# Performance work log

Measured on AMD Instinct MI355X. Metric: run time of the kernel, lower is better.

## Reference

```python
import jax, jax.numpy as jnp
import numpy as np

EMBED_DIM = 1024
NUM_HEADS = 16
D_K = EMBED_DIM // NUM_HEADS


def setup_inputs() -> dict:
    key = jax.random.key(0)
    ks = jax.random.split(key, 5)
    x = jax.random.normal(ks[0], (2, 2048, EMBED_DIM), dtype=jnp.float32)
    # kaiming_normal on 2D params: std = sqrt(2/fan_in) with fan_in = in_features
    w_qkv = jax.random.normal(ks[1], (3 * EMBED_DIM, EMBED_DIM), dtype=jnp.float32) * np.sqrt(2.0 / EMBED_DIM)
    b_qkv = jnp.zeros((3 * EMBED_DIM,), dtype=jnp.float32)
    w_o = jax.random.normal(ks[2], (EMBED_DIM, EMBED_DIM), dtype=jnp.float32) * np.sqrt(2.0 / EMBED_DIM)
    b_o = jnp.zeros((EMBED_DIM,), dtype=jnp.float32)
    return {"x": x, "w_qkv": w_qkv, "b_qkv": b_qkv, "w_o": w_o, "b_o": b_o}


def reference(x, w_qkv, b_qkv, w_o, b_o):
    B, N, C = x.shape
    qkv = x @ w_qkv.T + b_qkv  # [B,N,3C]
    q, k, v = jnp.split(qkv, 3, axis=-1)
    # [B,H,N,d_k]
    q = q.reshape(B, N, NUM_HEADS, D_K).transpose(0, 2, 1, 3)
    k = k.reshape(B, N, NUM_HEADS, D_K).transpose(0, 2, 1, 3)
    v = v.reshape(B, N, NUM_HEADS, D_K).transpose(0, 2, 1, 3)
    # NOTE: original forward scales by 1/sqrt(embed_dim), not 1/sqrt(d_k)
    scores = jnp.einsum('bhqd,bhkd->bhqk', q, k) / np.sqrt(C).astype(np.float32)
    causal = jnp.tril(jnp.ones((N, N), dtype=bool))
    scores = jnp.where(causal, scores, -jnp.inf)
    attn = jax.nn.softmax(scores, axis=-1)
    out = jnp.einsum('bhqk,bhkd->bhqd', attn, v)  # [B,H,N,d_k]
    out = out.transpose(0, 2, 1, 3).reshape(B, N, C)
    return out @ w_o.T + b_o
```

## Files before the change

kernel.cpp:

```cpp
#include <hip/hip_runtime.h>
#include <hip/hip_bf16.h>
#include <math.h>

typedef __bf16 bf16_t;
typedef __bf16 bf16x8 __attribute__((ext_vector_type(8)));
typedef __bf16 bf16x4 __attribute__((ext_vector_type(4)));
typedef __bf16 bf16x2 __attribute__((ext_vector_type(2)));
typedef float f32x4 __attribute__((ext_vector_type(4)));
typedef unsigned u32x4 __attribute__((ext_vector_type(4)));

#define SCALE_L2E 0.045084234f
#define ROUND_B 0.0028169f

#define MFMA16(a, b, c) __builtin_amdgcn_mfma_f32_16x16x32_bf16(a, b, c, 0, 0, 0)

__device__ __forceinline__ unsigned pack2(float a, float b) {
  return __builtin_amdgcn_perm(__builtin_bit_cast(unsigned, b),
                               __builtin_bit_cast(unsigned, a), 0x07060302u);
}

__global__ void convert3_f32_bf16(const float* __restrict__ a, int na,
                                  const float* __restrict__ b, int nb,
                                  const float* __restrict__ c, int nc,
                                  bf16_t* __restrict__ oa, bf16_t* __restrict__ ob,
                                  bf16_t* __restrict__ oc) {
  int i = (blockIdx.x * blockDim.x + threadIdx.x) * 8;
  const float* src;
  bf16_t* dst;
  int off;
  if (i < na) { src = a; dst = oa; off = i; }
  else if (i < na + nb) { src = b; dst = ob; off = i - na; }
  else if (i < na + nb + nc) { src = c; dst = oc; off = i - na - nb; }
  else return;
  float4 u = *(const float4*)&src[off];
  float4 v = *(const float4*)&src[off + 4];
  bf16x8 w = {(bf16_t)u.x, (bf16_t)u.y, (bf16_t)u.z, (bf16_t)u.w,
              (bf16_t)v.x, (bf16_t)v.y, (bf16_t)v.z, (bf16_t)v.w};
  *(bf16x8*)&dst[off] = w;
}

#define GLOBAL_AS __attribute__((address_space(1)))
#define LDS_AS __attribute__((address_space(3)))
__device__ __forceinline__ void g2l16(const void* g, void* l) {
  __builtin_amdgcn_global_load_lds((const GLOBAL_AS void*)g, (LDS_AS void*)l,
                                   16, 0, 0);
}

template <typename TC, int BN>
__launch_bounds__(256)
__global__ void gemm_bt_bias(const bf16_t* __restrict__ A,
                             const bf16_t* __restrict__ B,
                             const float* __restrict__ bias,
                             TC* __restrict__ C,
                             int M, int N, int K) {
  constexpr int NT = BN / 32;
  __shared__ bf16_t As[128 * 32];
  __shared__ bf16_t Bs[BN * 32];

  const int t = threadIdx.x;
  const int wave = t >> 6, lane = t & 63, quad = lane >> 4, ln = lane & 15;
  const int wm = (wave >> 1) * 64, wn = (wave & 1) * (BN / 2);
  const int m0 = blockIdx.y * 128, n0 = blockIdx.x * BN;

  const int srow = lane >> 2;
  const int schunk = ((lane & 3) ^ ((lane >> 3) & 3)) * 8;
  const bf16_t* gA0 = &A[(size_t)(m0 + wave * 32 + srow) * K + schunk];
  const bf16_t* gA1 = gA0 + (size_t)16 * K;
  bf16_t* lA0 = &As[(wave * 32) * 32];
  bf16_t* lA1 = &As[(wave * 32 + 16) * 32];
  const bf16_t* gB0 = &B[(size_t)(n0 + (BN == 128 ? wave * 32 : wave * 16) + srow) * K + schunk];
  const bf16_t* gB1 = gB0 + (size_t)16 * K;
  bf16_t* lB0 = &Bs[((BN == 128 ? wave * 32 : wave * 16)) * 32];
  bf16_t* lB1 = &Bs[(wave * 32 + 16) * 32];

  const int cslot = (quad ^ ((ln >> 1) & 3)) * 8;

  f32x4 acc[4][NT];
  for (int i = 0; i < 4; i++)
    for (int j = 0; j < NT; j++) acc[i][j] = (f32x4){0.f, 0.f, 0.f, 0.f};

  for (int k0 = 0; k0 < K; k0 += 32) {
    __syncthreads();
    g2l16(gA0 + k0, lA0);
    g2l16(gA1 + k0, lA1);
    g2l16(gB0 + k0, lB0);
    if (BN == 128) g2l16(gB1 + k0, lB1);
    __syncthreads();

    bf16x8 af[4], bfr[NT];
    for (int mt = 0; mt < 4; mt++)
      af[mt] = *(const bf16x8*)&As[(wm + mt * 16 + ln) * 32 + cslot];
    for (int nt = 0; nt < NT; nt++)
      bfr[nt] = *(const bf16x8*)&Bs[(wn + nt * 16 + ln) * 32 + cslot];
    for (int mt = 0; mt < 4; mt++)
      for (int nt = 0; nt < NT; nt++)
        acc[mt][nt] = MFMA16(af[mt], bfr[nt], acc[mt][nt]);
  }

  for (int nt = 0; nt < NT; nt++) {
    int col = n0 + wn + nt * 16 + ln;
    float bv = bias[col];
    for (int mt = 0; mt < 4; mt++) {
      int row = m0 + wm + mt * 16 + quad * 4;
      for (int r = 0; r < 4; r++)
        C[(size_t)(row + r) * N + col] = (TC)(acc[mt][nt][r] + bv);
    }
  }
}

__launch_bounds__(256, 2)
__global__ void attn_kernel(const bf16_t* __restrict__ qkv,
                            bf16_t* __restrict__ out) {
  constexpr int KP = 72, VP = 72;
  constexpr int BUF = 64 * KP;
  __shared__ __align__(16) bf16_t KsB[2 * BUF];
  __shared__ __align__(16) bf16_t VtB[2 * BUF];

  const int t = threadIdx.x;
  const int wave = t >> 6, lane = t & 63, quad = lane >> 4, ln = lane & 15;
  const int p = blockIdx.x & 15;
  const int bh = blockIdx.x >> 4;
  const int b = bh >> 4, h = bh & 15;
  const int qA = p * 64, qB = (31 - p) * 64;
  const int ntiles = 32 - p;
  const size_t rs = 3072;
  const size_t base = (size_t)b * 2048 * rs;

  const size_t qoffA = base + (size_t)(qA + wave * 16 + ln) * rs + h * 64;
  const size_t qoffB = base + (size_t)(qB + wave * 16 + ln) * rs + h * 64;
  bf16x8 qfA0 = *(const bf16x8*)&qkv[qoffA + quad * 8];
  bf16x8 qfA1 = *(const bf16x8*)&qkv[qoffA + 32 + quad * 8];
  bf16x8 qfB0 = *(const bf16x8*)&qkv[qoffB + quad * 8];
  bf16x8 qfB1 = *(const bf16x8*)&qkv[qoffB + 32 + quad * 8];

  f32x4 oA[4], oB[4];
  float lAx = 0.f, lBx = 0.f;
  for (int ct = 0; ct < 4; ct++) {
    oA[ct] = (f32x4){0.f, 0.f, 0.f, 0.f};
    oB[ct] = (f32x4){0.f, 0.f, 0.f, 0.f};
  }

  const int r0 = t >> 3, c0 = (t & 7) * 8;
  const int ksA = r0 * KP + (((t & 7) + wave) & 7) * 8;
  const int ksB2 = (r0 + 32) * KP + (((t & 7) + wave + 4) & 7) * 8;
  const int vkoff = ((((r0 >> 2) + (t & 7)) & 7)) * 8 + 2 * (r0 & 3);

  const bf16_t* kpa = &qkv[base + 1024 + h * 64 + (size_t)r0 * rs + c0];
  const bf16_t* kpb = kpa + (size_t)32 * rs;
  const bf16_t* vpa = &qkv[base + 2048 + h * 64 + (size_t)(2 * r0) * rs + c0];
  const bf16_t* vpb = vpa + rs;
  const size_t tstep = (size_t)64 * rs;

  bf16x8 ka = *(const bf16x8*)kpa; kpa += tstep;
  bf16x8 kb = *(const bf16x8*)kpb; kpb += tstep;
  bf16x8 va2 = *(const bf16x8*)vpa; vpa += tstep;
  bf16x8 vb2 = *(const bf16x8*)vpb; vpb += tstep;

  const int qgA = qA + wave * 16 + ln;
  const int qgB = qB + wave * 16 + ln;

  auto stage_to = [&](int buf) {
    bf16_t* KsW = &KsB[buf * BUF];
    bf16_t* VtW = &VtB[buf * BUF];
    *(bf16x8*)&KsW[ksA] = ka;
    *(bf16x8*)&KsW[ksB2] = kb;
#pragma unroll
    for (int j = 0; j < 8; j++) {
      bf16x2 w2 = {va2[j], vb2[j]};
      *(bf16x2*)&VtW[(c0 + j) * VP + vkoff] = w2;
    }
  };
  auto prefetch = [&]() {
    ka = *(const bf16x8*)kpa; kpa += tstep;
    kb = *(const bf16x8*)kpb; kpb += tstep;
    va2 = *(const bf16x8*)vpa; vpa += tstep;
    vb2 = *(const bf16x8*)vpb; vpb += tstep;
  };
  auto load_kfs = [&](const bf16_t* Ks, bf16x8* kf0s, bf16x8* kf1s) {
#pragma unroll
    for (int st = 0; st < 4; st++) {
      const int krow = st * 16 + ln;
      const int rot = 2 * st + (ln >> 3);
      kf0s[st] = *(const bf16x8*)&Ks[krow * KP + ((quad + rot) & 7) * 8];
      kf1s[st] = *(const bf16x8*)&Ks[krow * KP + ((quad + 4 + rot) & 7) * 8];
    }
  };
  auto qk_block = [&](const bf16x8* kf0s, const bf16x8* kf1s, bf16x8 q0,
                      bf16x8 q1, float& lx, bf16x8* Bp, bool masked,
                      int kbase, int qg) {
#pragma unroll
    for (int pr = 0; pr < 2; pr++) {
      u32x4 u;
#pragma unroll
      for (int sh = 0; sh < 2; sh++) {
        const int st = pr * 2 + sh;
        f32x4 s = (f32x4){0.f, 0.f, 0.f, 0.f};
        s = MFMA16(kf0s[st], q0, s);
        s = MFMA16(kf1s[st], q1, s);
        const int k0g = kbase + st * 16 + quad * 4;
        float pv[4];
#pragma unroll
        for (int r = 0; r < 4; r++) {
          float e = __builtin_amdgcn_exp2f(fmaf(s[r], SCALE_L2E, ROUND_B));
          if (masked && (k0g + r > qg)) e = 0.f;
          lx += e;
          pv[r] = e;
        }
        u[sh * 2] = pack2(pv[0], pv[1]);
        u[sh * 2 + 1] = pack2(pv[2], pv[3]);
      }
      Bp[pr] = __builtin_bit_cast(bf16x8, u);
    }
  };
  auto load_vfs = [&](const bf16_t* Vt, bf16x8* A8s) {
#pragma unroll
    for (int pr = 0; pr < 2; pr++) {
#pragma unroll
      for (int ct = 0; ct < 4; ct++) {
        const int dd = ct * 16 + ln;
        const int bc = (quad >> 1) + 2 * ct + (ln >> 3);
        const int cA = (4 * pr + bc) & 7;
        const int cB = (4 * pr + 2 + bc) & 7;
        bf16x4 v0 = *(const bf16x4*)&Vt[dd * VP + cA * 8 + (quad & 1) * 4];
        bf16x4 v1 = *(const bf16x4*)&Vt[dd * VP + cB * 8 + (quad & 1) * 4];
        A8s[pr * 4 + ct] = __builtin_shufflevector(v0, v1, 0, 1, 2, 3, 4, 5, 6, 7);
      }
    }
  };

  auto body = [&](int kt, bool hasA, bool maskA, bool maskB) {
    if (kt + 1 < ntiles) {
      stage_to((kt + 1) & 1);
      if (kt + 2 < ntiles) prefetch();
    }
    const bf16_t* Ks = &KsB[(kt & 1) * BUF];
    const bf16_t* Vt = &VtB[(kt & 1) * BUF];
    bf16x8 kf0s[4], kf1s[4];
    load_kfs(Ks, kf0s, kf1s);
    bf16x8 BpA[2], BpB[2];
    if (hasA) qk_block(kf0s, kf1s, qfA0, qfA1, lAx, BpA, maskA, kt * 64, qgA);
    qk_block(kf0s, kf1s, qfB0, qfB1, lBx, BpB, maskB, kt * 64, qgB);
    bf16x8 A8s[8];
    load_vfs(Vt, A8s);
#pragma unroll
    for (int pr = 0; pr < 2; pr++) {
#pragma unroll
      for (int ct = 0; ct < 4; ct++) {
        if (hasA) oA[ct] = MFMA16(A8s[pr * 4 + ct], BpA[pr], oA[ct]);
        oB[ct] = MFMA16(A8s[pr * 4 + ct], BpB[pr], oB[ct]);
      }
    }
    if (kt + 1 < ntiles) __syncthreads();
  };

  stage_to(0);
  if (ntiles > 1) prefetch();
  __syncthreads();

  for (int kt = 0; kt < p; kt++) body(kt, true, false, false);
  body(p, true, true, false);
  for (int kt = p + 1; kt < 31 - p; kt++) body(kt, false, false, false);
  body(31 - p, false, false, true);

  lAx += __shfl_xor(lAx, 16);
  lAx += __shfl_xor(lAx, 32);
  lBx += __shfl_xor(lBx, 16);
  lBx += __shfl_xor(lBx, 32);
  const float invA = __builtin_amdgcn_rcpf(lAx);
  const float invB = __builtin_amdgcn_rcpf(lBx);
  const int ocol = h * 64 + quad * 4;
#pragma unroll
  for (int ct = 0; ct < 4; ct++) {
    bf16x4 wa, wb;
#pragma unroll
    for (int r = 0; r < 4; r++) {
      wa[r] = (bf16_t)(oA[ct][r] * invA);
      wb[r] = (bf16_t)(oB[ct][r] * invB);
    }
    *(bf16x4*)&out[(size_t)(b * 2048 + qgA) * 1024 + ocol + ct * 16] = wa;
    *(bf16x4*)&out[(size_t)(b * 2048 + qgB) * 1024 + ocol + ct * 16] = wb;
  }
}

extern "C" void kernel_launch(void* const* d_in, const int* in_sizes, int n_in,
                              void* d_out, int out_size, void* d_ws, size_t ws_size,
                              hipStream_t stream) {
  const float* x     = (const float*)d_in[0];
  const float* w_qkv = (const float*)d_in[1];
  const float* b_qkv = (const float*)d_in[2];
  const float* w_o   = (const float*)d_in[3];
  const float* b_o   = (const float*)d_in[4];
  float* out = (float*)d_out;

  bf16_t* qkv   = (bf16_t*)d_ws;
  bf16_t* xbf   = qkv + (size_t)4096 * 3072;
  bf16_t* wqkvb = xbf + (size_t)4096 * 1024;
  bf16_t* wob   = wqkvb + (size_t)3072 * 1024;
  bf16_t* attn  = xbf;

  const int na = 4096 * 1024, nb = 3072 * 1024, nc = 1024 * 1024;
  convert3_f32_bf16<<<dim3((na + nb + nc) / (256 * 8)), 256, 0, stream>>>(
      x, na, w_qkv, nb, w_o, nc, xbf, wqkvb, wob);

  gemm_bt_bias<bf16_t, 128><<<dim3(3072 / 128, 4096 / 128), 256, 0, stream>>>(
      xbf, wqkvb, b_qkv, qkv, 4096, 3072, 1024);
  attn_kernel<<<dim3(512), 256, 0, stream>>>(qkv, attn);
  gemm_bt_bias<float, 64><<<dim3(1024 / 64, 4096 / 128), 256, 0, stream>>>(
      attn, wob, b_o, out, 4096, 1024, 1024);
}
```

Measured before the change: 179.1 us.

## Add 256x256-tile pipelined QKV GEMM with swizzled LDS and phased MFMA

Replaces the 128x128-tile QKV projection GEMM with a new 512-thread kernel that computes 256x256 output tiles. It double-buffers 64-wide K slices in LDS using XOR-swizzled layouts and splits each K step into four sub-phases that interleave global-to-LDS loads with MFMA bursts, raising wave priority around the math. The aim is more data reuse per tile and better overlap of memory traffic with compute. The cost is heavy LDS use (128 KB per block) and only 192 blocks, which may underfill the GPU's compute units and limit occupancy.

```diff
diff --git a/kernel.cpp b/kernel.cpp
--- a/kernel.cpp
+++ b/kernel.cpp
@@ -108,6 +108,134 @@
   }
 }
 
+__launch_bounds__(512, 2)
+__global__ void gemm256_bt_bias(const bf16_t* __restrict__ A,
+                                const bf16_t* __restrict__ B,
+                                const float* __restrict__ bias,
+                                bf16_t* __restrict__ C,
+                                int M, int N, int K) {
+  __shared__ __align__(16) bf16_t Ab[2][256 * 64];
+  __shared__ __align__(16) bf16_t Bb[2][256 * 64];
+
+  const int tid = threadIdx.x;
+  const int wave = tid >> 6, lane = tid & 63, quad = lane >> 4, ln = lane & 15;
+  const int wm = wave >> 2, wn = wave & 3;
+  const int m0 = blockIdx.y * 256, n0 = blockIdx.x * 256;
+  const int nt = K >> 6;
+
+  const int rowoff = wave * 8 + (lane >> 3);
+  const int c8 = ((lane & 7) ^ (lane >> 3)) * 8;
+  const int w8row = wave * 8;
+  const bf16_t* Arow0 = A + (size_t)(m0 + rowoff) * K + c8;
+  const bf16_t* Brow0 = B + (size_t)(n0 + rowoff) * K + c8;
+
+  auto stA = [&](int tl, int h) {
+    const bf16_t* g = Arow0 + (size_t)(h * 128) * K + (size_t)tl * 64;
+    bf16_t* l = &Ab[tl & 1][(h * 128 + w8row) * 64];
+    g2l16(g, l);
+    g2l16(g + (size_t)64 * K, l + 64 * 64);
+  };
+  auto stB = [&](int tl, int h) {
+    const bf16_t* g = Brow0 + (size_t)(h * 128) * K + (size_t)tl * 64;
+    bf16_t* l = &Bb[tl & 1][(h * 128 + w8row) * 64];
+    g2l16(g, l);
+    g2l16(g + (size_t)64 * K, l + 64 * 64);
+  };
+
+  const int cswl = (quad ^ (ln & 7)) * 8;
+  const int aBase = (wm * 64 + ln) * 64;
+  const int bBase = (wn * 32 + ln) * 64;
+
+  f32x4 acc[8][4];
+#pragma unroll
+  for (int i = 0; i < 8; i++)
+#pragma unroll
+    for (int j = 0; j < 4; j++) acc[i][j] = (f32x4){0.f, 0.f, 0.f, 0.f};
+
+  bf16x8 af[4][2], bfr[2][2];
+
+  auto ldA4 = [&](int buf, int mh) {
+#pragma unroll
+    for (int mf = 0; mf < 4; ++mf)
+#pragma unroll
+      for (int sk = 0; sk < 2; ++sk)
+        af[mf][sk] = *(const bf16x8*)&Ab[buf][mh * 8192 + aBase + mf * 1024 +
+                                             (cswl ^ (sk << 5))];
+  };
+  auto ldB2 = [&](int buf, int nh) {
+#pragma unroll
+    for (int nf = 0; nf < 2; ++nf)
+#pragma unroll
+      for (int sk = 0; sk < 2; ++sk)
+        bfr[nf][sk] = *(const bf16x8*)&Bb[buf][nh * 8192 + bBase + nf * 1024 +
+                                               (cswl ^ (sk << 5))];
+  };
+  auto mm8 = [&](int mh, int nh) {
+#pragma unroll
+    for (int mf = 0; mf < 4; ++mf)
+#pragma unroll
+      for (int nf = 0; nf < 2; ++nf) {
+        f32x4 c = acc[mh * 4 + mf][nh * 2 + nf];
+        c = MFMA16(af[mf][0], bfr[nf][0], c);
+        c = MFMA16(af[mf][1], bfr[nf][1], c);
+        acc[mh * 4 + mf][nh * 2 + nf] = c;
+      }
+  };
+
+#define PHASE_MM(MH, NH)                             \
+  __builtin_amdgcn_s_barrier();                      \
+  asm volatile("s_waitcnt lgkmcnt(0)" ::: "memory"); \
+  __builtin_amdgcn_s_setprio(1);                     \
+  mm8(MH, NH);                                       \
+  __builtin_amdgcn_s_setprio(0);
+
+  stA(0, 0); stB(0, 0); stA(0, 1); stB(0, 1);
+  if (nt > 1) {
+    stA(1, 0); stB(1, 0);
+    asm volatile("s_waitcnt vmcnt(4)" ::: "memory");
+  } else {
+    asm volatile("s_waitcnt vmcnt(0)" ::: "memory");
+  }
+  __builtin_amdgcn_s_barrier();
+
+  for (int tl = 0; tl < nt; ++tl) {
+    const int buf = tl & 1;
+    ldA4(buf, 0);
+    ldB2(buf, 0);
+    if (tl + 1 < nt) stA(tl + 1, 1);
+    PHASE_MM(0, 0)
+    __builtin_amdgcn_s_barrier();
+    ldB2(buf, 1);
+    if (tl + 1 < nt) stB(tl + 1, 1);
+    PHASE_MM(0, 1)
+    __builtin_amdgcn_s_barrier();
+    ldA4(buf, 1);
+    ldB2(buf, 0);
+    if (tl + 2 < nt) stA(tl + 2, 0);
+    PHASE_MM(1, 0)
+    __builtin_amdgcn_s_barrier();
+    ldB2(buf, 1);
+    if (tl + 2 < nt) stB(tl + 2, 0);
+    PHASE_MM(1, 1)
+    asm volatile("s_waitcnt vmcnt(4)" ::: "memory");
+    __builtin_amdgcn_s_barrier();
+  }
+#undef PHASE_MM
+
+#pragma unroll
+  for (int nf4 = 0; nf4 < 4; ++nf4) {
+    const int col = n0 + (nf4 >> 1) * 128 + wn * 32 + (nf4 & 1) * 16 + ln;
+    const float bv = bias[col];
+#pragma unroll
+    for (int mf8 = 0; mf8 < 8; ++mf8) {
+      const int row = m0 + (mf8 >> 2) * 128 + wm * 64 + (mf8 & 3) * 16 + quad * 4;
+#pragma unroll
+      for (int r = 0; r < 4; ++r)
+        C[(size_t)(row + r) * N + col] = (bf16_t)(acc[mf8][nf4][r] + bv);
+    }
+  }
+}
+
 __launch_bounds__(256, 2)
 __global__ void attn_kernel(const bf16_t* __restrict__ qkv,
                             bf16_t* __restrict__ out) {
@@ -302,7 +430,7 @@
   convert3_f32_bf16<<<dim3((na + nb + nc) / (256 * 8)), 256, 0, stream>>>(
       x, na, w_qkv, nb, w_o, nc, xbf, wqkvb, wob);
 
-  gemm_bt_bias<bf16_t, 128><<<dim3(3072 / 128, 4096 / 128), 256, 0, stream>>>(
+  gemm256_bt_bias<<<dim3(3072 / 256, 4096 / 256), 512, 0, stream>>>(
       xbf, wqkvb, b_qkv, qkv, 4096, 3072, 1024);
   attn_kernel<<<dim3(512), 256, 0, stream>>>(qkv, attn);
   gemm_bt_bias<float, 64><<<dim3(1024 / 64, 4096 / 128), 256, 0, stream>>>(
```

New measurement: 176.3 us. No clear change (-1.6%).
